# Kernel optimization log

Hardware: AMD Instinct MI355X
Metric: run time of the kernel (lower is better)

The kernel has to match this reference:

```python
import jax, jax.numpy as jnp
import numpy as np

C, L, N, D, V = 8, 4096, 4096, 128, 100000

def setup_inputs() -> dict:
    key = jax.random.key(0)
    k1, k2, k3, k4 = jax.random.split(key, 4)
    ngram_seq = jax.random.randint(k1, (C, N), 0, V, dtype=jnp.int64)
    hidden_state = jax.random.normal(k2, (L, D), dtype=jnp.float32)
    word_ngram_mask_matrix = jax.random.uniform(k3, (C, L, N), dtype=jnp.float32)
    channel_ids = jnp.arange(C, dtype=jnp.int64)
    W_emb = jax.random.normal(k4, (V, D), dtype=jnp.float32)
    W_emb = W_emb.at[0].set(0.0)  # padding_idx=0
    W_channel = jax.random.normal(jax.random.fold_in(key, 5), (C, 1), dtype=jnp.float32)
    return {"ngram_seq": ngram_seq, "hidden_state": hidden_state,
            "word_ngram_mask_matrix": word_ngram_mask_matrix,
            "channel_ids": channel_ids, "W_emb": W_emb, "W_channel": W_channel}

def reference(ngram_seq, hidden_state, word_ngram_mask_matrix, channel_ids, W_emb, W_channel):
    temper = jnp.float32(np.sqrt(D))
    emb = W_emb[ngram_seq]                                   # [C, N, D]
    # u = (emb @ hidden^T)/temper, then permute -> [C, L, N]
    u = jnp.einsum('cnd,ld->cln', emb, hidden_state) / temper
    mask = jnp.clip(word_ngram_mask_matrix, 0.0, 1.0)        # [C, L, N]
    delta_exp_u = jnp.exp(u) * mask                          # masked exp (no max-shift, as in source)
    attention = delta_exp_u / (jnp.sum(delta_exp_u, axis=2, keepdims=True) + 1e-10)
    character_attention = jnp.einsum('cln,cnd->cld', attention, emb)  # [C, L, D]
    channel_w = W_channel[channel_ids]                       # [C, 1]
    channel_w = jax.nn.softmax(channel_w, axis=1)            # trivial over size-1 dim, kept for fidelity
    character_attention = character_attention * channel_w.reshape(-1, 1, 1)
    out = jnp.transpose(character_attention, (1, 0, 2)).reshape(L, C * D)  # [L, C*D]
    return out
```

## Files before the change

kernel.cpp:

```cpp
#include <hip/hip_runtime.h>


typedef __bf16 bf16_t;
typedef bf16_t bf16x8 __attribute__((ext_vector_type(8)));
typedef bf16_t bf16x4 __attribute__((ext_vector_type(4)));
typedef bf16_t bf16x2 __attribute__((ext_vector_type(2)));
typedef float  f32x16 __attribute__((ext_vector_type(16)));
typedef float  f32x4  __attribute__((ext_vector_type(4)));

#define C_ 8
#define L_ 4096
#define N_ 4096
#define D_ 128

__global__ __launch_bounds__(512) void ngram_attn_kernel(
    const int* __restrict__ seq,
    const float* __restrict__ hidden,
    const float* __restrict__ mask,
    const float* __restrict__ Wemb,
    float* __restrict__ out)
{
  __shared__ bf16_t Hs [128][136];
  __shared__ bf16_t End[128][136];
  __shared__ bf16_t Et [128][136];
  __shared__ bf16_t Ps [128][136];
  __shared__ float  dpart[4][128];
  __shared__ float  dinv[128];

  const int bid  = blockIdx.x;
  const int c    = bid & 7;
  const int l0   = (bid >> 3) * 128;
  const int tid  = threadIdx.x;
  const int wv   = tid >> 6;
  const int lane = tid & 63;
  const int mrow = lane & 31;
  const int hi   = lane >> 5;
  const int nb   = wv & 3;
  const int lh   = wv >> 2;

  const float inv_temper = 0.08838834764831845f;

  #pragma unroll
  for (int rep = 0; rep < 8; ++rep) {
    int u = tid + rep * 512;
    int q = u & 31, r = u >> 5;
    f32x4 h4 = *(const f32x4*)(hidden + (size_t)(l0 + r) * D_ + q * 4);
    bf16x4 hb = { (bf16_t)h4[0], (bf16_t)h4[1], (bf16_t)h4[2], (bf16_t)h4[3] };
    *(bf16x4*)&Hs[r][q * 4] = hb;
  }

  f32x16 Oacc0, Oacc1;
  #pragma unroll
  for (int i = 0; i < 16; ++i) { Oacc0[i] = 0.f; Oacc1[i] = 0.f; }
  float dsum0 = 0.f, dsum1 = 0.f;

  const int* seq_c = seq + (size_t)c * N_;

  #pragma unroll 1
  for (int nt = 0; nt < 32; ++nt) {
    const int n0 = nt * 128;
    __syncthreads();

    #pragma unroll
    for (int rep = 0; rep < 2; ++rep) {
      int u  = tid + rep * 512;
      int np = u & 63, g = u >> 6;
      int n1 = 2 * np, n2 = n1 + 1;
      int i1 = seq_c[n0 + n1], i2 = seq_c[n0 + n2];
      const f32x4* r1 = (const f32x4*)(Wemb + (size_t)i1 * D_ + g * 8);
      const f32x4* r2 = (const f32x4*)(Wemb + (size_t)i2 * D_ + g * 8);
      f32x4 a0 = r1[0], a1 = r1[1];
      f32x4 b0 = r2[0], b1 = r2[1];
      bf16x8 e1 = { (bf16_t)a0[0], (bf16_t)a0[1], (bf16_t)a0[2], (bf16_t)a0[3],
                    (bf16_t)a1[0], (bf16_t)a1[1], (bf16_t)a1[2], (bf16_t)a1[3] };
      bf16x8 e2 = { (bf16_t)b0[0], (bf16_t)b0[1], (bf16_t)b0[2], (bf16_t)b0[3],
                    (bf16_t)b1[0], (bf16_t)b1[1], (bf16_t)b1[2], (bf16_t)b1[3] };
      *(bf16x8*)&End[n1][g * 8] = e1;
      *(bf16x8*)&End[n2][g * 8] = e2;
      #pragma unroll
      for (int i = 0; i < 8; ++i) {
        bf16x2 t = { e1[i], e2[i] };
        *(bf16x2*)&Et[g * 8 + i][n1] = t;
      }
    }
    __syncthreads();

    f32x4 mreg[2][4];
    #pragma unroll
    for (int cb = 0; cb < 2; ++cb) {
      int lg = l0 + lh * 64 + cb * 32 + mrow;
      const float* mp = mask + ((size_t)c * L_ + lg) * N_ + n0 + nb * 32 + 4 * hi;
      #pragma unroll
      for (int g = 0; g < 4; ++g)
        mreg[cb][g] = *(const f32x4*)(mp + 8 * g);
    }

    f32x16 S0, S1;
    #pragma unroll
    for (int i = 0; i < 16; ++i) { S0[i] = 0.f; S1[i] = 0.f; }
    #pragma unroll
    for (int ks = 0; ks < 8; ++ks) {
      bf16x8 a = *(const bf16x8*)&End[nb * 32 + mrow][ks * 16 + hi * 8];
      bf16x8 b0 = *(const bf16x8*)&Hs[lh * 64 + 0  + mrow][ks * 16 + hi * 8];
      bf16x8 b1 = *(const bf16x8*)&Hs[lh * 64 + 32 + mrow][ks * 16 + hi * 8];
      S0 = __builtin_amdgcn_mfma_f32_32x32x16_bf16(a, b0, S0, 0, 0, 0);
      S1 = __builtin_amdgcn_mfma_f32_32x32x16_bf16(a, b1, S1, 0, 0, 0);
    }

    #pragma unroll
    for (int cb = 0; cb < 2; ++cb) {
      int lrow = lh * 64 + cb * 32 + mrow;
      #pragma unroll
      for (int g = 0; g < 4; ++g) {
        bf16x4 pw;
        float lsum = 0.f;
        #pragma unroll
        for (int j = 0; j < 4; ++j) {
          float s = (cb == 0) ? S0[4 * g + j] : S1[4 * g + j];
          float m = mreg[cb][g][j];
          m = fminf(fmaxf(m, 0.f), 1.f);
          float wval = __expf(s * inv_temper) * m;
          lsum += wval;
          pw[j] = (bf16_t)wval;
        }
        if (cb == 0) dsum0 += lsum; else dsum1 += lsum;
        *(bf16x4*)&Ps[lrow][nb * 32 + 8 * g + 4 * hi] = pw;
      }
    }
    __syncthreads();

    #pragma unroll
    for (int ks = 0; ks < 8; ++ks) {
      bf16x8 a = *(const bf16x8*)&Ps[nb * 32 + mrow][ks * 16 + hi * 8];
      bf16x8 b0 = *(const bf16x8*)&Et[lh * 64 + 0  + mrow][ks * 16 + hi * 8];
      bf16x8 b1 = *(const bf16x8*)&Et[lh * 64 + 32 + mrow][ks * 16 + hi * 8];
      Oacc0 = __builtin_amdgcn_mfma_f32_32x32x16_bf16(a, b0, Oacc0, 0, 0, 0);
      Oacc1 = __builtin_amdgcn_mfma_f32_32x32x16_bf16(a, b1, Oacc1, 0, 0, 0);
    }
  }

  {
    float v0 = dsum0 + __shfl_xor(dsum0, 32, 64);
    float v1 = dsum1 + __shfl_xor(dsum1, 32, 64);
    if (hi == 0) {
      dpart[nb][lh * 64 + 0  + mrow] = v0;
      dpart[nb][lh * 64 + 32 + mrow] = v1;
    }
  }
  __syncthreads();
  if (tid < 128) {
    float s = dpart[0][tid] + dpart[1][tid] + dpart[2][tid] + dpart[3][tid] + 1e-10f;
    dinv[tid] = 1.0f / s;
  }
  __syncthreads();

  #pragma unroll
  for (int r = 0; r < 16; ++r) {
    int row  = (r & 3) + 8 * (r >> 2) + 4 * hi;
    int lloc = nb * 32 + row;
    float inv = dinv[lloc];
    size_t base = (size_t)(l0 + lloc) * (C_ * D_) + c * D_ + lh * 64 + mrow;
    out[base]      = Oacc0[r] * inv;
    out[base + 32] = Oacc1[r] * inv;
  }
}

extern "C" void kernel_launch(void* const* d_in, const int* in_sizes, int n_in,
                              void* d_out, int out_size, void* d_ws, size_t ws_size,
                              hipStream_t stream) {
  (void)in_sizes; (void)n_in; (void)out_size; (void)d_ws; (void)ws_size;
  const int*   seq    = (const int*)d_in[0];
  const float* hidden = (const float*)d_in[1];
  const float* mask   = (const float*)d_in[2];
  const float* Wemb   = (const float*)d_in[4];
  float* out = (float*)d_out;
  ngram_attn_kernel<<<dim3(256), dim3(512), 0, stream>>>(seq, hidden, mask, Wemb, out);
}
```

Before: 847.3 us.

## Prefetch next tile's embeddings and mask into registers, keep hidden in registers

```diff
diff --git a/kernel.cpp b/kernel.cpp
--- a/kernel.cpp
+++ b/kernel.cpp
@@ -3,7 +3,6 @@
 
 typedef __bf16 bf16_t;
 typedef bf16_t bf16x8 __attribute__((ext_vector_type(8)));
-typedef bf16_t bf16x4 __attribute__((ext_vector_type(4)));
 typedef bf16_t bf16x2 __attribute__((ext_vector_type(2)));
 typedef float  f32x16 __attribute__((ext_vector_type(16)));
 typedef float  f32x4  __attribute__((ext_vector_type(4)));
@@ -13,18 +12,17 @@
 #define N_ 4096
 #define D_ 128
 
-__global__ __launch_bounds__(512) void ngram_attn_kernel(
+__global__ __launch_bounds__(512, 2) void ngram_attn_kernel(
     const int* __restrict__ seq,
     const float* __restrict__ hidden,
     const float* __restrict__ mask,
     const float* __restrict__ Wemb,
     float* __restrict__ out)
 {
-  __shared__ bf16_t Hs [128][136];
   __shared__ bf16_t End[128][136];
   __shared__ bf16_t Et [128][136];
   __shared__ bf16_t Ps [128][136];
-  __shared__ float  dpart[4][128];
+  __shared__ float  dpart[2][128];
   __shared__ float  dinv[128];
 
   const int bid  = blockIdx.x;
@@ -35,42 +33,78 @@
   const int lane = tid & 63;
   const int mrow = lane & 31;
   const int hi   = lane >> 5;
-  const int nb   = wv & 3;
-  const int lh   = wv >> 2;
+  const int lsl  = wv & 3;
+  const int nh   = wv >> 2;
 
   const float inv_temper = 0.08838834764831845f;
-
+  const int* seq_c = seq + (size_t)c * N_;
+
+  bf16x8 Ha[8];
+  {
+    const float* hrow = hidden + (size_t)(l0 + lsl * 32 + mrow) * D_ + hi * 8;
+    #pragma unroll
+    for (int ks = 0; ks < 8; ++ks) {
+      f32x4 h0 = *(const f32x4*)(hrow + ks * 16);
+      f32x4 h1 = *(const f32x4*)(hrow + ks * 16 + 4);
+      Ha[ks] = (bf16x8){ (bf16_t)h0[0], (bf16_t)h0[1], (bf16_t)h0[2], (bf16_t)h0[3],
+                         (bf16_t)h1[0], (bf16_t)h1[1], (bf16_t)h1[2], (bf16_t)h1[3] };
+    }
+  }
+
+  const int lrow_base = lsl * 32 + 4 * hi;
+  const int ncol      = nh * 64 + mrow;
+  const float* mrow_base = mask + ((size_t)c * L_ + l0 + lrow_base) * N_ + ncol;
+
+  int   sidxB[4];
+  f32x4 ereg[8];
+  float mreg[32];
+
+  {
+    int sidxA[4];
+    #pragma unroll
+    for (int rep = 0; rep < 2; ++rep) {
+      int u = tid + rep * 512, np = u & 63;
+      sidxA[2 * rep + 0] = seq_c[2 * np];
+      sidxA[2 * rep + 1] = seq_c[2 * np + 1];
+    }
+    #pragma unroll
+    for (int rep = 0; rep < 2; ++rep) {
+      int u = tid + rep * 512, g = u >> 6;
+      const f32x4* r1 = (const f32x4*)(Wemb + (size_t)sidxA[2 * rep + 0] * D_ + g * 8);
+      const f32x4* r2 = (const f32x4*)(Wemb + (size_t)sidxA[2 * rep + 1] * D_ + g * 8);
+      ereg[4 * rep + 0] = r1[0]; ereg[4 * rep + 1] = r1[1];
+      ereg[4 * rep + 2] = r2[0]; ereg[4 * rep + 3] = r2[1];
+    }
+    #pragma unroll
+    for (int rep = 0; rep < 2; ++rep) {
+      int u = tid + rep * 512, np = u & 63;
+      sidxB[2 * rep + 0] = seq_c[128 + 2 * np];
+      sidxB[2 * rep + 1] = seq_c[128 + 2 * np + 1];
+    }
+    #pragma unroll
+    for (int r = 0; r < 16; ++r) {
+      const float* mp = mrow_base + (size_t)((r & 3) + 8 * (r >> 2)) * N_;
+      mreg[2 * r + 0] = __builtin_nontemporal_load(mp);
+      mreg[2 * r + 1] = __builtin_nontemporal_load(mp + 32);
+    }
+  }
+
+  f32x16 Oacc0, Oacc1;
+  float dacc[16];
   #pragma unroll
-  for (int rep = 0; rep < 8; ++rep) {
-    int u = tid + rep * 512;
-    int q = u & 31, r = u >> 5;
-    f32x4 h4 = *(const f32x4*)(hidden + (size_t)(l0 + r) * D_ + q * 4);
-    bf16x4 hb = { (bf16_t)h4[0], (bf16_t)h4[1], (bf16_t)h4[2], (bf16_t)h4[3] };
-    *(bf16x4*)&Hs[r][q * 4] = hb;
-  }
-
-  f32x16 Oacc0, Oacc1;
-  #pragma unroll
-  for (int i = 0; i < 16; ++i) { Oacc0[i] = 0.f; Oacc1[i] = 0.f; }
-  float dsum0 = 0.f, dsum1 = 0.f;
-
-  const int* seq_c = seq + (size_t)c * N_;
+  for (int i = 0; i < 16; ++i) { Oacc0[i] = 0.f; Oacc1[i] = 0.f; dacc[i] = 0.f; }
 
   #pragma unroll 1
   for (int nt = 0; nt < 32; ++nt) {
-    const int n0 = nt * 128;
     __syncthreads();
 
     #pragma unroll
     for (int rep = 0; rep < 2; ++rep) {
-      int u  = tid + rep * 512;
+      int u = tid + rep * 512;
       int np = u & 63, g = u >> 6;
       int n1 = 2 * np, n2 = n1 + 1;
-      int i1 = seq_c[n0 + n1], i2 = seq_c[n0 + n2];
-      const f32x4* r1 = (const f32x4*)(Wemb + (size_t)i1 * D_ + g * 8);
-      const f32x4* r2 = (const f32x4*)(Wemb + (size_t)i2 * D_ + g * 8);
-      f32x4 a0 = r1[0], a1 = r1[1];
-      f32x4 b0 = r2[0], b1 = r2[1];
+      f32x4 a0 = ereg[4 * rep + 0], a1 = ereg[4 * rep + 1];
+      f32x4 b0 = ereg[4 * rep + 2], b1 = ereg[4 * rep + 3];
       bf16x8 e1 = { (bf16_t)a0[0], (bf16_t)a0[1], (bf16_t)a0[2], (bf16_t)a0[3],
                     (bf16_t)a1[0], (bf16_t)a1[1], (bf16_t)a1[2], (bf16_t)a1[3] };
       bf16x8 e2 = { (bf16_t)b0[0], (bf16_t)b0[1], (bf16_t)b0[2], (bf16_t)b0[3],
@@ -85,83 +119,95 @@
     }
     __syncthreads();
 
-    f32x4 mreg[2][4];
-    #pragma unroll
-    for (int cb = 0; cb < 2; ++cb) {
-      int lg = l0 + lh * 64 + cb * 32 + mrow;
-      const float* mp = mask + ((size_t)c * L_ + lg) * N_ + n0 + nb * 32 + 4 * hi;
-      #pragma unroll
-      for (int g = 0; g < 4; ++g)
-        mreg[cb][g] = *(const f32x4*)(mp + 8 * g);
-    }
-
     f32x16 S0, S1;
     #pragma unroll
     for (int i = 0; i < 16; ++i) { S0[i] = 0.f; S1[i] = 0.f; }
     #pragma unroll
     for (int ks = 0; ks < 8; ++ks) {
-      bf16x8 a = *(const bf16x8*)&End[nb * 32 + mrow][ks * 16 + hi * 8];
-      bf16x8 b0 = *(const bf16x8*)&Hs[lh * 64 + 0  + mrow][ks * 16 + hi * 8];
-      bf16x8 b1 = *(const bf16x8*)&Hs[lh * 64 + 32 + mrow][ks * 16 + hi * 8];
-      S0 = __builtin_amdgcn_mfma_f32_32x32x16_bf16(a, b0, S0, 0, 0, 0);
-      S1 = __builtin_amdgcn_mfma_f32_32x32x16_bf16(a, b1, S1, 0, 0, 0);
-    }
-
-    #pragma unroll
-    for (int cb = 0; cb < 2; ++cb) {
-      int lrow = lh * 64 + cb * 32 + mrow;
-      #pragma unroll
-      for (int g = 0; g < 4; ++g) {
-        bf16x4 pw;
-        float lsum = 0.f;
-        #pragma unroll
-        for (int j = 0; j < 4; ++j) {
-          float s = (cb == 0) ? S0[4 * g + j] : S1[4 * g + j];
-          float m = mreg[cb][g][j];
-          m = fminf(fmaxf(m, 0.f), 1.f);
-          float wval = __expf(s * inv_temper) * m;
-          lsum += wval;
-          pw[j] = (bf16_t)wval;
-        }
-        if (cb == 0) dsum0 += lsum; else dsum1 += lsum;
-        *(bf16x4*)&Ps[lrow][nb * 32 + 8 * g + 4 * hi] = pw;
+      bf16x8 b0 = *(const bf16x8*)&End[nh * 64 + 0  + mrow][ks * 16 + hi * 8];
+      bf16x8 b1 = *(const bf16x8*)&End[nh * 64 + 32 + mrow][ks * 16 + hi * 8];
+      S0 = __builtin_amdgcn_mfma_f32_32x32x16_bf16(Ha[ks], b0, S0, 0, 0, 0);
+      S1 = __builtin_amdgcn_mfma_f32_32x32x16_bf16(Ha[ks], b1, S1, 0, 0, 0);
+    }
+
+    {
+      int ntp = (nt < 31) ? nt + 1 : 31;
+      #pragma unroll
+      for (int rep = 0; rep < 2; ++rep) {
+        int u = tid + rep * 512, g = u >> 6;
+        const f32x4* r1 = (const f32x4*)(Wemb + (size_t)sidxB[2 * rep + 0] * D_ + g * 8);
+        const f32x4* r2 = (const f32x4*)(Wemb + (size_t)sidxB[2 * rep + 1] * D_ + g * 8);
+        ereg[4 * rep + 0] = r1[0]; ereg[4 * rep + 1] = r1[1];
+        ereg[4 * rep + 2] = r2[0]; ereg[4 * rep + 3] = r2[1];
+      }
+      int nts = (nt < 30) ? nt + 2 : 31;
+      const int* sp = seq_c + nts * 128;
+      #pragma unroll
+      for (int rep = 0; rep < 2; ++rep) {
+        int u = tid + rep * 512, np = u & 63;
+        sidxB[2 * rep + 0] = sp[2 * np];
+        sidxB[2 * rep + 1] = sp[2 * np + 1];
+      }
+      (void)ntp;
+    }
+
+    #pragma unroll
+    for (int r = 0; r < 16; ++r) {
+      int lr = lsl * 32 + (r & 3) + 8 * (r >> 2) + 4 * hi;
+      float m0 = fminf(fmaxf(mreg[2 * r + 0], 0.f), 1.f);
+      float m1 = fminf(fmaxf(mreg[2 * r + 1], 0.f), 1.f);
+      float w0 = __expf(S0[r] * inv_temper) * m0;
+      float w1 = __expf(S1[r] * inv_temper) * m1;
+      dacc[r] += w0 + w1;
+      Ps[lr][nh * 64 + mrow]      = (bf16_t)w0;
+      Ps[lr][nh * 64 + 32 + mrow] = (bf16_t)w1;
+    }
+
+    {
+      int ntp = (nt < 31) ? nt + 1 : 31;
+      const float* mb = mrow_base + (size_t)ntp * 128;
+      #pragma unroll
+      for (int r = 0; r < 16; ++r) {
+        const float* mp = mb + (size_t)((r & 3) + 8 * (r >> 2)) * N_;
+        mreg[2 * r + 0] = __builtin_nontemporal_load(mp);
+        mreg[2 * r + 1] = __builtin_nontemporal_load(mp + 32);
       }
     }
     __syncthreads();
 
     #pragma unroll
     for (int ks = 0; ks < 8; ++ks) {
-      bf16x8 a = *(const bf16x8*)&Ps[nb * 32 + mrow][ks * 16 + hi * 8];
-      bf16x8 b0 = *(const bf16x8*)&Et[lh * 64 + 0  + mrow][ks * 16 + hi * 8];
-      bf16x8 b1 = *(const bf16x8*)&Et[lh * 64 + 32 + mrow][ks * 16 + hi * 8];
+      bf16x8 a  = *(const bf16x8*)&Ps[lsl * 32 + mrow][ks * 16 + hi * 8];
+      bf16x8 b0 = *(const bf16x8*)&Et[nh * 64 + 0  + mrow][ks * 16 + hi * 8];
+      bf16x8 b1 = *(const bf16x8*)&Et[nh * 64 + 32 + mrow][ks * 16 + hi * 8];
       Oacc0 = __builtin_amdgcn_mfma_f32_32x32x16_bf16(a, b0, Oacc0, 0, 0, 0);
       Oacc1 = __builtin_amdgcn_mfma_f32_32x32x16_bf16(a, b1, Oacc1, 0, 0, 0);
     }
   }
 
-  {
-    float v0 = dsum0 + __shfl_xor(dsum0, 32, 64);
-    float v1 = dsum1 + __shfl_xor(dsum1, 32, 64);
-    if (hi == 0) {
-      dpart[nb][lh * 64 + 0  + mrow] = v0;
-      dpart[nb][lh * 64 + 32 + mrow] = v1;
-    }
-  }
-  __syncthreads();
-  if (tid < 128) {
-    float s = dpart[0][tid] + dpart[1][tid] + dpart[2][tid] + dpart[3][tid] + 1e-10f;
-    dinv[tid] = 1.0f / s;
-  }
-  __syncthreads();
-
   #pragma unroll
   for (int r = 0; r < 16; ++r) {
-    int row  = (r & 3) + 8 * (r >> 2) + 4 * hi;
-    int lloc = nb * 32 + row;
-    float inv = dinv[lloc];
-    size_t base = (size_t)(l0 + lloc) * (C_ * D_) + c * D_ + lh * 64 + mrow;
-    out[base]      = Oacc0[r] * inv;
-    out[base + 32] = Oacc1[r] * inv;
+    float v = dacc[r];
+    v += __shfl_xor(v, 1, 64);
+    v += __shfl_xor(v, 2, 64);
+    v += __shfl_xor(v, 4, 64);
+    v += __shfl_xor(v, 8, 64);
+    v += __shfl_xor(v, 16, 64);
+    if (mrow == 0)
+      dpart[nh][lsl * 32 + (r & 3) + 8 * (r >> 2) + 4 * hi] = v;
+  }
+  __syncthreads();
+  if (tid < 128)
+    dinv[tid] = 1.0f / (dpart[0][tid] + dpart[1][tid] + 1e-10f);
+  __syncthreads();
+
+  #pragma unroll
+  for (int r = 0; r < 16; ++r) {
+    int lr = lsl * 32 + (r & 3) + 8 * (r >> 2) + 4 * hi;
+    float inv = dinv[lr];
+    size_t base = (size_t)(l0 + lr) * (C_ * D_) + c * D_ + nh * 64 + mrow;
+    __builtin_nontemporal_store(Oacc0[r] * inv, out + base);
+    __builtin_nontemporal_store(Oacc1[r] * inv, out + base + 32);
   }
 }
 
```

Measured after the change: 830.7 us. No clear change (-2.0%).
